# Optimization experiments

Measured on AMD Instinct MI355X. Metric: run time of the kernel, lower is better.

The kernel has to match this reference:

```python
import jax, jax.numpy as jnp
import numpy as np

B, N, DIN, A = 64, 64, 64, 32
DOUT = 128          # obs_output_dim == obs_act_output_dim == 128 (required by module wiring)
OA_IN = DIN + A     # obs_act_input_dim = 96


def _w(key, shape):
    fan_in = shape[-1]
    return jax.random.normal(key, shape, jnp.float32) / jnp.sqrt(jnp.float32(fan_in))


def setup_inputs() -> dict:
    key = jax.random.key(0)
    ks = jax.random.split(key, 14)
    return {
        "states": jax.random.normal(ks[0], (B, N, DIN), jnp.float32),
        "policies": jax.random.uniform(ks[1], (B, N, A), jnp.float32),
        "actions": jax.random.uniform(ks[2], (B, N, A), jnp.float32),
        # state_embed_preproc: Linear(obs_input_dim, 128) + LeakyReLU
        "W_se_pre": _w(ks[3], (128, DIN)),
        "b_se_pre": jnp.zeros((128,), jnp.float32),
        # key/query layers (shared between both attention stages in forward)
        "W_key": _w(ks[4], (DOUT, 128)),
        "W_query": _w(ks[5], (DOUT, 128)),
        # state_embed: Linear(obs_output_dim, 128) + LeakyReLU
        "W_se": _w(ks[6], (128, DOUT)),
        "b_se": jnp.zeros((128,), jnp.float32),
        # state_act_pol_embed: Linear(obs_act_input_dim, 128) + LeakyReLU
        "W_sap": _w(ks[7], (128, OA_IN)),
        "b_sap": jnp.zeros((128,), jnp.float32),
        # attention_value_layer: Linear(128, obs_act_output_dim)
        "W_av": _w(ks[8], (DOUT, 128)),
        # final value head
        "W_f1": _w(ks[9], (64, DOUT)),
        "W_f2": _w(ks[10], (1, 64)),
    }


def reference(states, policies, actions, W_se_pre, b_se_pre, W_key, W_query,
              W_se, b_se, W_sap, b_sap, W_av, W_f1, W_f2):
    lrelu = jax.nn.leaky_relu  # negative_slope=0.01, matches torch default
    d_k = W_key.shape[0]
    inv_sqrt_dk = 1.0 / jnp.sqrt(jnp.asarray(d_k, states.dtype))

    # stage 1: self-attention over agents on raw-state embeddings
    e = lrelu(states @ W_se_pre.T + b_se_pre)                       # [B,N,128]
    q1 = e @ W_query.T
    k1 = e @ W_key.T
    w_pre = jax.nn.softmax(jnp.einsum('bid,bjd->bij', q1, k1) * inv_sqrt_dk, axis=-1)
    # NB: attention_value_layer_preproc output is overwritten in the original forward;
    # the effective value is weight_preproc @ states_embed_preproc.
    av_pre = jnp.einsum('bij,bjd->bid', w_pre, e)                   # [B,N,128]

    # stage 2: self-attention weights over agents on re-embedded states
    se = lrelu(av_pre @ W_se.T + b_se)                              # [B,N,128]
    q2 = se @ W_query.T
    k2 = se @ W_key.T
    w = jax.nn.softmax(jnp.einsum('bid,bjd->bij', q2, k2) * inv_sqrt_dk, axis=-1)

    # obs_actions_policies[b,j,k] = (state_k, policy_k) if j==k else (state_k, action_k)
    obs_act = jnp.concatenate([states, actions], axis=-1)           # [B,N,OA_IN]
    obs_pol = jnp.concatenate([states, policies], axis=-1)
    n = states.shape[1]
    eye = jnp.eye(n, dtype=states.dtype)[None, :, :, None]          # [1,N,N,1]
    oap = eye * obs_pol[:, None, :, :] + (1.0 - eye) * obs_act[:, None, :, :]  # [B,N,N,OA_IN]

    emb = lrelu(oap @ W_sap.T + b_sap)                              # [B,N,N,128]
    av = emb @ W_av.T                                               # [B,N,N,DOUT]

    # fused form of repeat->weight->sum: node[b,i,j,d] = sum_k w[b,i,k] * av[b,j,k,d]
    node = jnp.einsum('bik,bjkd->bijd', w, av)                      # [B,N,N,DOUT]

    value = lrelu(node @ W_f1.T) @ W_f2.T                           # [B,N,N,1]
    return value, w_pre, w
```

## Files before the change

### kernel.cpp

```cpp
#include <hip/hip_runtime.h>

#define DEVFN __device__ __forceinline__

constexpr int BNN = 64 * 64 * 64;
constexpr float SCALE = 0.08838834764831845f;
constexpr float NSLOPE = 0.01f;

constexpr int OFF_WPRET = 0;
constexpr int OFF_M     = 24576;
constexpr int OFF_WSET  = 40960;
constexpr int OFF_WSAPT = 57344;
constexpr int OFF_WAVT  = 69632;
constexpr int OFF_WF1T  = 86016;
constexpr int OFF_E     = 98304;
constexpr int OFF_Q     = 622592;
constexpr int OFF_ET    = 1146880;
constexpr int OFF_SET   = 1671168;
constexpr int OFF_HA    = 2195456;
constexpr int OFF_HD    = 2719744;


DEVFN void fma4(float (&acc)[4], float a, const float4& bv) {
  acc[0] += a * bv.x; acc[1] += a * bv.y; acc[2] += a * bv.z; acc[3] += a * bv.w;
}
DEVFN void fma2(float (&acc)[2], float a, const float2& bv) {
  acc[0] += a * bv.x; acc[1] += a * bv.y;
}


template<int NT>
DEVFN void st128(int tid, const float* __restrict__ src, float* __restrict__ Bs, int rows) {
  const int n4 = rows * 32;
  for (int idx = tid; idx < n4; idx += NT) {
    const int r = idx >> 5, c = idx & 31;
    *reinterpret_cast<float4*>(&Bs[r * 132 + c * 4]) =
        *reinterpret_cast<const float4*>(&src[r * 128 + c * 4]);
  }
}

template<int NT>
DEVFN void st64r(int tid, const float* __restrict__ src, float* __restrict__ Bs, int rows) {
  const int n4 = rows * 16;
  for (int idx = tid; idx < n4; idx += NT) {
    const int r = idx >> 4, c = idx & 15;
    *reinterpret_cast<float4*>(&Bs[r * 68 + c * 4]) =
        *reinterpret_cast<const float4*>(&src[r * 64 + c * 4]);
  }
}

DEVFN void wrT(int tid, const float* __restrict__ S, float* __restrict__ dst, int rq) {
  const int fr = tid >> 2, a4 = tid & 3;
  float t[4];
#pragma unroll
  for (int i = 0; i < 4; ++i) t[i] = S[(a4 * 4 + i) * 132 + fr];
  float4 v; v.x = t[0]; v.y = t[1]; v.z = t[2]; v.w = t[3];
  *reinterpret_cast<float4*>(&dst[fr * 64 + rq * 16 + a4 * 4]) = v;
}


DEVFN void g1(int tid, const float* __restrict__ A, int lda,
              const float* __restrict__ Bs, int K, float (&acc)[4]) {
  const int c0 = (tid & 31) * 4, rg = tid >> 5;
  const float* __restrict__ Ar = A + rg * lda;
#pragma unroll 4
  for (int k4 = 0; k4 < K; k4 += 4) {
    const float4 a4 = *reinterpret_cast<const float4*>(&Ar[k4]);
    const float4 b0 = *reinterpret_cast<const float4*>(&Bs[(k4 + 0) * 132 + c0]);
    const float4 b1 = *reinterpret_cast<const float4*>(&Bs[(k4 + 1) * 132 + c0]);
    const float4 b2 = *reinterpret_cast<const float4*>(&Bs[(k4 + 2) * 132 + c0]);
    const float4 b3 = *reinterpret_cast<const float4*>(&Bs[(k4 + 3) * 132 + c0]);
    fma4(acc, a4.x, b0); fma4(acc, a4.y, b1); fma4(acc, a4.z, b2); fma4(acc, a4.w, b3);
  }
}

DEVFN void g2A(int tid, const float* __restrict__ A0, const float* __restrict__ A1,
               int lda, const float* __restrict__ Bs, int K,
               float (&a0)[4], float (&a1)[4]) {
  const int c0 = (tid & 31) * 4, rg = tid >> 5;
  const float* __restrict__ X = A0 + rg * lda;
  const float* __restrict__ Y = A1 + rg * lda;
#pragma unroll 2
  for (int k4 = 0; k4 < K; k4 += 4) {
    const float4 x4 = *reinterpret_cast<const float4*>(&X[k4]);
    const float4 y4 = *reinterpret_cast<const float4*>(&Y[k4]);
    const float4 b0 = *reinterpret_cast<const float4*>(&Bs[(k4 + 0) * 132 + c0]);
    const float4 b1 = *reinterpret_cast<const float4*>(&Bs[(k4 + 1) * 132 + c0]);
    const float4 b2 = *reinterpret_cast<const float4*>(&Bs[(k4 + 2) * 132 + c0]);
    const float4 b3 = *reinterpret_cast<const float4*>(&Bs[(k4 + 3) * 132 + c0]);
    fma4(a0, x4.x, b0); fma4(a1, y4.x, b0);
    fma4(a0, x4.y, b1); fma4(a1, y4.y, b1);
    fma4(a0, x4.z, b2); fma4(a1, y4.z, b2);
    fma4(a0, x4.w, b3); fma4(a1, y4.w, b3);
  }
}

DEVFN void gH(int tid, const float* __restrict__ A, int lda,
              const float* __restrict__ Bs, int K, float (&acc)[2]) {
  const int c0 = (tid & 31) * 2, rg = tid >> 5;
  const float* __restrict__ Ar = A + rg * lda;
#pragma unroll 4
  for (int k4 = 0; k4 < K; k4 += 4) {
    const float4 a4 = *reinterpret_cast<const float4*>(&Ar[k4]);
    const float2 b0 = *reinterpret_cast<const float2*>(&Bs[(k4 + 0) * 68 + c0]);
    const float2 b1 = *reinterpret_cast<const float2*>(&Bs[(k4 + 1) * 68 + c0]);
    const float2 b2 = *reinterpret_cast<const float2*>(&Bs[(k4 + 2) * 68 + c0]);
    const float2 b3 = *reinterpret_cast<const float2*>(&Bs[(k4 + 3) * 68 + c0]);
    fma2(acc, a4.x, b0); fma2(acc, a4.y, b1); fma2(acc, a4.z, b2); fma2(acc, a4.w, b3);
  }
}

DEVFN void gH2(int tid, const float* __restrict__ A0, const float* __restrict__ A1,
               int lda, const float* __restrict__ Bs, int K,
               float (&a0)[2], float (&a1)[2]) {
  const int c0 = (tid & 31) * 2, rg = tid >> 5;
  const float* __restrict__ X = A0 + rg * lda;
  const float* __restrict__ Y = A1 + rg * lda;
#pragma unroll 2
  for (int k4 = 0; k4 < K; k4 += 4) {
    const float4 x4 = *reinterpret_cast<const float4*>(&X[k4]);
    const float4 y4 = *reinterpret_cast<const float4*>(&Y[k4]);
    const float2 b0 = *reinterpret_cast<const float2*>(&Bs[(k4 + 0) * 68 + c0]);
    const float2 b1 = *reinterpret_cast<const float2*>(&Bs[(k4 + 1) * 68 + c0]);
    const float2 b2 = *reinterpret_cast<const float2*>(&Bs[(k4 + 2) * 68 + c0]);
    const float2 b3 = *reinterpret_cast<const float2*>(&Bs[(k4 + 3) * 68 + c0]);
    fma2(a0, x4.x, b0); fma2(a1, y4.x, b0);
    fma2(a0, x4.y, b1); fma2(a1, y4.y, b1);
    fma2(a0, x4.z, b2); fma2(a1, y4.z, b2);
    fma2(a0, x4.w, b3); fma2(a1, y4.w, b3);
  }
}

template<bool ACT, bool HASB>
DEVFN void epi(int tid, const float (&acc)[4], float* __restrict__ O, int ldo,
               const float* __restrict__ bias) {
  const int c0 = (tid & 31) * 4, rg = tid >> 5;
  float t[4];
#pragma unroll
  for (int i = 0; i < 4; ++i) {
    float x = acc[i];
    if constexpr (HASB) x += bias[c0 + i];
    if constexpr (ACT) x = (x > 0.f) ? x : NSLOPE * x;
    t[i] = x;
  }
  float4 v; v.x = t[0]; v.y = t[1]; v.z = t[2]; v.w = t[3];
  *reinterpret_cast<float4*>(&O[rg * ldo + c0]) = v;
}


DEVFN void score_full(int tid, const float* __restrict__ Qs,
                      const float* __restrict__ Ks, float (&acc)[2]) {
  const int j = tid & 63, iw = tid >> 6;
#pragma unroll 2
  for (int kt = 0; kt < 128; kt += 8) {
    float qv[2][8];
#pragma unroll
    for (int r = 0; r < 2; ++r) {
      *reinterpret_cast<float4*>(&qv[r][0]) =
          *reinterpret_cast<const float4*>(&Qs[(iw * 2 + r) * 132 + kt]);
      *reinterpret_cast<float4*>(&qv[r][4]) =
          *reinterpret_cast<const float4*>(&Qs[(iw * 2 + r) * 132 + kt + 4]);
    }
#pragma unroll
    for (int kk = 0; kk < 8; ++kk) {
      const float kv = Ks[(kt + kk) * 68 + j];
      acc[0] += qv[0][kk] * kv;
      acc[1] += qv[1][kk] * kv;
    }
  }
}

DEVFN void softmax_write(int tid, float (&acc)[2], float* __restrict__ Wp,
                         float* __restrict__ gout) {
  const int j = tid & 63, iw = tid >> 6;
#pragma unroll
  for (int r = 0; r < 2; ++r) {
    float v = acc[r] * SCALE;
    float m = v;
#pragma unroll
    for (int off = 32; off > 0; off >>= 1) m = fmaxf(m, __shfl_xor(m, off, 64));
    const float p = __expf(v - m);
    float s = p;
#pragma unroll
    for (int off = 32; off > 0; off >>= 1) s += __shfl_xor(s, off, 64);
    const float w = p / s;
    Wp[(iw * 2 + r) * 68 + j] = w;
    gout[(iw * 2 + r) * 64 + j] = w;
  }
}


__global__ __launch_bounds__(512) void WPREP(const float* __restrict__ Wpre,
                                             const float* __restrict__ Wq,
                                             const float* __restrict__ Wkey,
                                             const float* __restrict__ Wse,
                                             const float* __restrict__ Wsap,
                                             const float* __restrict__ Wav,
                                             const float* __restrict__ Wf1,
                                             float* __restrict__ ws) {
  __shared__ float As[16 * 132];
  __shared__ float Bs[64 * 132];
  const int tid = threadIdx.x, bid = blockIdx.x;
  if (bid < 120) {
    const int gt = bid * 512 + tid;
    if (gt < 8192) {
      const int c = gt >> 6, k = gt & 63;
      ws[OFF_WPRET + k * 128 + c] = Wpre[gt];
    } else if (gt < 24576) {
      const int i = gt - 8192, c = i >> 7, k = i & 127;
      ws[OFF_WSET + k * 128 + c] = Wse[i];
    } else if (gt < 36864) {
      const int i = gt - 24576, c = i / 96, k = i - c * 96;
      ws[OFF_WSAPT + k * 128 + c] = Wsap[i];
    } else if (gt < 53248) {
      const int i = gt - 36864, c = i >> 7, k = i & 127;
      ws[OFF_WAVT + k * 128 + c] = Wav[i];
    } else if (gt < 61440) {
      const int i = gt - 53248, c = i >> 7, k = i & 127;
      ws[OFF_WF1T + k * 64 + c] = Wf1[i];
    }
  } else {
    const int r0 = (bid - 120) * 16;
    for (int idx = tid; idx < 2048; idx += 512) {
      const int r = idx & 15, o = idx >> 4;
      As[r * 132 + o] = Wq[o * 128 + r0 + r];
    }
    const int c0 = (tid & 31) * 4, rg = tid >> 5;
    float acc[4] = {};
    for (int h = 0; h < 2; ++h) {
      __syncthreads();
      st128<512>(tid, Wkey + h * 8192, Bs, 64);
      __syncthreads();
#pragma unroll 8
      for (int k = 0; k < 64; ++k) {
        const float4 bv = *reinterpret_cast<const float4*>(&Bs[k * 132 + c0]);
        fma4(acc, As[rg * 132 + h * 64 + k], bv);
      }
    }
    float4 v; v.x = acc[0]; v.y = acc[1]; v.z = acc[2]; v.w = acc[3];
    *reinterpret_cast<float4*>(&ws[OFF_M + (r0 + rg) * 128 + c0]) = v;
  }
}

__global__ __launch_bounds__(512) void P1(const float* __restrict__ states,
                                          const float* __restrict__ policies,
                                          const float* __restrict__ actions,
                                          const float* __restrict__ b_sap,
                                          const float* __restrict__ b_se_pre,
                                          float* __restrict__ ws) {
  __shared__ float S[16 * 68];
  __shared__ float Aa[16 * 36], Ap[16 * 36];
  __shared__ float Ea[16 * 132];
  __shared__ float Ep[16 * 132], Dd[16 * 132], Er[16 * 132];
  __shared__ float Bs[8704];
  const int tid = threadIdx.x;
  const int wid = ((blockIdx.x & 7) << 5) | (blockIdx.x >> 3);
  const int b = wid >> 2, rq = wid & 3;
  const int r0g = b * 64 + rq * 16;

  for (int idx = tid; idx < 1024; idx += 512) {
    const int r = idx >> 6, c = idx & 63;
    S[r * 68 + c] = states[(r0g + r) * 64 + c];
  }
  {
    const int r = tid >> 5, c = tid & 31;
    Aa[r * 36 + c] = actions[(r0g + r) * 32 + c];
    Ap[r * 36 + c] = policies[(r0g + r) * 32 + c];
  }
  st128<512>(tid, ws + OFF_WSAPT, Bs, 64);
  __syncthreads();
  float cm[4] = {};
  g1(tid, S, 68, Bs, 64, cm);
  __syncthreads();
  st128<512>(tid, ws + OFF_WSAPT + 8192, Bs, 32);
  __syncthreads();
  float aa[4] = {cm[0], cm[1], cm[2], cm[3]};
  float ap[4] = {cm[0], cm[1], cm[2], cm[3]};
  g2A(tid, Aa, Ap, 36, Bs, 32, aa, ap);
  epi<true, true>(tid, aa, Ea, 132, b_sap);
  epi<true, true>(tid, ap, Ep, 132, b_sap);
  __syncthreads();
  for (int idx = tid; idx < 2048; idx += 512) {
    const int r = idx >> 7, c = idx & 127;
    Ep[r * 132 + c] -= Ea[r * 132 + c];
  }
  __syncthreads();
  st128<512>(tid, ws + OFF_WAVT, Bs, 64);
  __syncthreads();
  float av[4] = {}, dl[4] = {};
  g2A(tid, Ea, Ep, 132, Bs, 64, av, dl);
  __syncthreads();
  st128<512>(tid, ws + OFF_WAVT + 8192, Bs, 64);
  __syncthreads();
  g2A(tid, Ea + 64, Ep + 64, 132, Bs, 64, av, dl);
  __syncthreads();
  epi<false, false>(tid, av, Ea, 132, nullptr);
  epi<false, false>(tid, dl, Dd, 132, nullptr);
  __syncthreads();
  st64r<512>(tid, ws + OFF_WF1T, Bs, 128);
  __syncthreads();
  float ah[2] = {}, aha[2] = {};
  gH2(tid, Dd, Ea, 132, Bs, 64, ah, aha);
  gH2(tid, Dd + 64, Ea + 64, 132, Bs + 64 * 68, 64, ah, aha);
  {
    const int c0 = (tid & 31) * 2, rg = tid >> 5;
    float2 vh; vh.x = ah[0]; vh.y = ah[1];
    float2 va; va.x = aha[0]; va.y = aha[1];
    *reinterpret_cast<float2*>(&ws[OFF_HD + (r0g + rg) * 64 + c0]) = vh;
    *reinterpret_cast<float2*>(&ws[OFF_HA + (r0g + rg) * 64 + c0]) = va;
  }
  __syncthreads();
  st128<512>(tid, ws + OFF_WPRET, Bs, 64);
  __syncthreads();
  {
    float ae[4] = {};
    g1(tid, S, 68, Bs, 64, ae);
    const int c0 = (tid & 31) * 4, rg = tid >> 5;
    float t[4];
#pragma unroll
    for (int i = 0; i < 4; ++i) {
      float x = ae[i] + b_se_pre[c0 + i];
      t[i] = (x > 0.f) ? x : NSLOPE * x;
    }
    float4 v; v.x = t[0]; v.y = t[1]; v.z = t[2]; v.w = t[3];
    *reinterpret_cast<float4*>(&Er[rg * 132 + c0]) = v;
    *reinterpret_cast<float4*>(&ws[OFF_E + (r0g + rg) * 128 + c0]) = v;
  }
  __syncthreads();
  wrT(tid, Er, ws + OFF_ET + b * 8192, rq);
  st128<512>(tid, ws + OFF_M, Bs, 64);
  __syncthreads();
  float af[4] = {};
  g1(tid, Er, 132, Bs, 64, af);
  __syncthreads();
  st128<512>(tid, ws + OFF_M + 8192, Bs, 64);
  __syncthreads();
  g1(tid, Er + 64, 132, Bs, 64, af);
  epi<false, false>(tid, af, ws + OFF_Q + r0g * 128, 128, nullptr);
}

__global__ __launch_bounds__(512) void P3(const float* __restrict__ b_se,
                                          float* __restrict__ ws,
                                          float* __restrict__ out) {
  __shared__ float Qs[16 * 132];
  __shared__ float Bs[8704];
  __shared__ float Wp[16 * 68], AV[16 * 132], SEr[16 * 132];
  const int tid = threadIdx.x;
  const int wid = ((blockIdx.x & 7) << 5) | (blockIdx.x >> 3);
  const int b = wid >> 2, rq = wid & 3;
  const int r0g = b * 64 + rq * 16;

  {
    const int r = tid >> 5, c = tid & 31;
    *reinterpret_cast<float4*>(&Qs[r * 132 + c * 4]) =
        *reinterpret_cast<const float4*>(&ws[OFF_Q + (r0g + r) * 128 + c * 4]);
  }
  st64r<512>(tid, ws + OFF_ET + b * 8192, Bs, 128);
  __syncthreads();
  float sc[2] = {};
  score_full(tid, Qs, Bs, sc);
  softmax_write(tid, sc, Wp, out + BNN + b * 4096 + rq * 1024);
  __syncthreads();
  st128<512>(tid, ws + OFF_E + b * 8192, Bs, 64);
  __syncthreads();
  {
    float a[4] = {};
    g1(tid, Wp, 68, Bs, 64, a);
    epi<false, false>(tid, a, AV, 132, nullptr);
  }
  __syncthreads();
  st128<512>(tid, ws + OFF_WSET, Bs, 64);
  __syncthreads();
  float as[4] = {};
  g1(tid, AV, 132, Bs, 64, as);
  __syncthreads();
  st128<512>(tid, ws + OFF_WSET + 8192, Bs, 64);
  __syncthreads();
  g1(tid, AV + 64, 132, Bs, 64, as);
  {
    const int c0 = (tid & 31) * 4, rg = tid >> 5;
    float t[4];
#pragma unroll
    for (int i = 0; i < 4; ++i) {
      float x = as[i] + b_se[c0 + i];
      t[i] = (x > 0.f) ? x : NSLOPE * x;
    }
    float4 v; v.x = t[0]; v.y = t[1]; v.z = t[2]; v.w = t[3];
    *reinterpret_cast<float4*>(&SEr[rg * 132 + c0]) = v;
  }
  __syncthreads();
  wrT(tid, SEr, ws + OFF_SET + b * 8192, rq);
  st128<512>(tid, ws + OFF_M, Bs, 64);
  __syncthreads();
  float af[4] = {};
  g1(tid, SEr, 132, Bs, 64, af);
  __syncthreads();
  st128<512>(tid, ws + OFF_M + 8192, Bs, 64);
  __syncthreads();
  g1(tid, SEr + 64, 132, Bs, 64, af);
  epi<false, false>(tid, af, ws + OFF_Q + r0g * 128, 128, nullptr);
}

__global__ __launch_bounds__(512) void P4(const float* __restrict__ Wf2g,
                                          float* __restrict__ ws,
                                          float* __restrict__ out) {
  __shared__ float Qs[16 * 132];
  __shared__ float Bs[8704];
  __shared__ float Wp[16 * 68], Hb[16 * 66];
  __shared__ float Hd[64 * 69];
  __shared__ float Wf2s[64];
  const int tid = threadIdx.x;
  const int wid = ((blockIdx.x & 7) << 5) | (blockIdx.x >> 3);
  const int b = wid >> 2, rq = wid & 3;
  const int r0g = b * 64 + rq * 16;

  for (int idx = tid; idx < 4096; idx += 512)
    Hd[(idx >> 6) * 69 + (idx & 63)] = ws[OFF_HD + b * 4096 + idx];
  if (tid < 64) Wf2s[tid] = Wf2g[tid];
  {
    const int r = tid >> 5, c = tid & 31;
    *reinterpret_cast<float4*>(&Qs[r * 132 + c * 4]) =
        *reinterpret_cast<const float4*>(&ws[OFF_Q + (r0g + r) * 128 + c * 4]);
  }
  st64r<512>(tid, ws + OFF_SET + b * 8192, Bs, 128);
  __syncthreads();
  float sc[2] = {};
  score_full(tid, Qs, Bs, sc);
  softmax_write(tid, sc, Wp, out + 2 * BNN + b * 4096 + rq * 1024);
  __syncthreads();
  st64r<512>(tid, ws + OFF_HA + b * 4096, Bs, 64);
  __syncthreads();
  float ah[2] = {};
  gH(tid, Wp, 68, Bs, 64, ah);
  {
    const int c0 = (tid & 31) * 2, rg = tid >> 5;
    float2 v; v.x = ah[0]; v.y = ah[1];
    *reinterpret_cast<float2*>(&Hb[rg * 66 + c0]) = v;
  }
  __syncthreads();
  const int j = tid & 63, iw = tid >> 6;
  float wv[2], a2[2] = {0.f, 0.f};
#pragma unroll
  for (int r = 0; r < 2; ++r) wv[r] = Wp[(iw * 2 + r) * 68 + j];
  for (int f = 0; f < 64; ++f) {
    const float hdv = Hd[j * 69 + f];
    const float wf = Wf2s[f];
#pragma unroll
    for (int r = 0; r < 2; ++r) {
      float t = Hb[(iw * 2 + r) * 66 + f] + wv[r] * hdv;
      t = (t > 0.f) ? t : NSLOPE * t;
      a2[r] += t * wf;
    }
  }
#pragma unroll
  for (int r = 0; r < 2; ++r)
    out[(r0g + iw * 2 + r) * 64 + j] = a2[r];
}

extern "C" void kernel_launch(void* const* d_in, const int* in_sizes, int n_in,
                              void* d_out, int out_size, void* d_ws, size_t ws_size,
                              hipStream_t stream) {
  const float* states   = (const float*)d_in[0];
  const float* policies = (const float*)d_in[1];
  const float* actions  = (const float*)d_in[2];
  const float* W_se_pre = (const float*)d_in[3];
  const float* b_se_pre = (const float*)d_in[4];
  const float* W_key    = (const float*)d_in[5];
  const float* W_query  = (const float*)d_in[6];
  const float* W_se     = (const float*)d_in[7];
  const float* b_se     = (const float*)d_in[8];
  const float* W_sap    = (const float*)d_in[9];
  const float* b_sap    = (const float*)d_in[10];
  const float* W_av     = (const float*)d_in[11];
  const float* W_f1     = (const float*)d_in[12];
  const float* W_f2     = (const float*)d_in[13];
  float* out = (float*)d_out;
  float* ws  = (float*)d_ws;

  WPREP<<<dim3(128), dim3(512), 0, stream>>>(
      W_se_pre, W_query, W_key, W_se, W_sap, W_av, W_f1, ws);
  P1<<<dim3(256), dim3(512), 0, stream>>>(states, policies, actions, b_sap, b_se_pre, ws);
  P3<<<dim3(256), dim3(512), 0, stream>>>(b_se, ws, out);
  P4<<<dim3(256), dim3(512), 0, stream>>>(W_f2, ws, out);
}
```

Measured before the change: 62.17 us.

## Fuse P3 and P4 kernels using per-batch atomic group barrier

Merges the second-stage attention kernel and the final value kernel into one launch. The four blocks of each batch synchronise through a global atomic counter, spinning until all four have written their transposed SE slice. Q2 now stays in shared memory instead of going through the workspace. This removes one kernel launch and a global round trip. In exchange it adds a memset launch and relies on all 256 blocks being co-resident, otherwise the spin wait can deadlock.

```diff
diff --git a/kernel.cpp b/kernel.cpp
--- a/kernel.cpp
+++ b/kernel.cpp
@@ -7,6 +7,7 @@
 constexpr float NSLOPE = 0.01f;
 
 constexpr int OFF_WPRET = 0;
+constexpr int OFF_CNT   = 8192;
 constexpr int OFF_M     = 24576;
 constexpr int OFF_WSET  = 40960;
 constexpr int OFF_WSAPT = 57344;
@@ -186,6 +187,17 @@
     Wp[(iw * 2 + r) * 68 + j] = w;
     gout[(iw * 2 + r) * 64 + j] = w;
   }
+}
+
+DEVFN void groupbar(unsigned* __restrict__ cnt, int tid) {
+  __syncthreads();
+  if (tid == 0) {
+    __hip_atomic_fetch_add(cnt, 1u, __ATOMIC_RELEASE, __HIP_MEMORY_SCOPE_AGENT);
+    while (__hip_atomic_load(cnt, __ATOMIC_ACQUIRE, __HIP_MEMORY_SCOPE_AGENT) < 4u) {
+      __builtin_amdgcn_s_sleep(2);
+    }
+  }
+  __syncthreads();
 }
 
 
@@ -338,94 +350,84 @@
   epi<false, false>(tid, af, ws + OFF_Q + r0g * 128, 128, nullptr);
 }
 
-__global__ __launch_bounds__(512) void P3(const float* __restrict__ b_se,
-                                          float* __restrict__ ws,
-                                          float* __restrict__ out) {
+__global__ __launch_bounds__(512) void P34(const float* __restrict__ b_se,
+                                           const float* __restrict__ Wf2g,
+                                           float* __restrict__ ws,
+                                           float* __restrict__ out) {
   __shared__ float Qs[16 * 132];
   __shared__ float Bs[8704];
-  __shared__ float Wp[16 * 68], AV[16 * 132], SEr[16 * 132];
-  const int tid = threadIdx.x;
-  const int wid = ((blockIdx.x & 7) << 5) | (blockIdx.x >> 3);
-  const int b = wid >> 2, rq = wid & 3;
-  const int r0g = b * 64 + rq * 16;
-
-  {
-    const int r = tid >> 5, c = tid & 31;
-    *reinterpret_cast<float4*>(&Qs[r * 132 + c * 4]) =
-        *reinterpret_cast<const float4*>(&ws[OFF_Q + (r0g + r) * 128 + c * 4]);
-  }
-  st64r<512>(tid, ws + OFF_ET + b * 8192, Bs, 128);
-  __syncthreads();
-  float sc[2] = {};
-  score_full(tid, Qs, Bs, sc);
-  softmax_write(tid, sc, Wp, out + BNN + b * 4096 + rq * 1024);
-  __syncthreads();
-  st128<512>(tid, ws + OFF_E + b * 8192, Bs, 64);
-  __syncthreads();
-  {
-    float a[4] = {};
-    g1(tid, Wp, 68, Bs, 64, a);
-    epi<false, false>(tid, a, AV, 132, nullptr);
-  }
-  __syncthreads();
-  st128<512>(tid, ws + OFF_WSET, Bs, 64);
-  __syncthreads();
-  float as[4] = {};
-  g1(tid, AV, 132, Bs, 64, as);
-  __syncthreads();
-  st128<512>(tid, ws + OFF_WSET + 8192, Bs, 64);
-  __syncthreads();
-  g1(tid, AV + 64, 132, Bs, 64, as);
-  {
-    const int c0 = (tid & 31) * 4, rg = tid >> 5;
-    float t[4];
-#pragma unroll
-    for (int i = 0; i < 4; ++i) {
-      float x = as[i] + b_se[c0 + i];
-      t[i] = (x > 0.f) ? x : NSLOPE * x;
-    }
-    float4 v; v.x = t[0]; v.y = t[1]; v.z = t[2]; v.w = t[3];
-    *reinterpret_cast<float4*>(&SEr[rg * 132 + c0]) = v;
-  }
-  __syncthreads();
-  wrT(tid, SEr, ws + OFF_SET + b * 8192, rq);
-  st128<512>(tid, ws + OFF_M, Bs, 64);
-  __syncthreads();
-  float af[4] = {};
-  g1(tid, SEr, 132, Bs, 64, af);
-  __syncthreads();
-  st128<512>(tid, ws + OFF_M + 8192, Bs, 64);
-  __syncthreads();
-  g1(tid, SEr + 64, 132, Bs, 64, af);
-  epi<false, false>(tid, af, ws + OFF_Q + r0g * 128, 128, nullptr);
-}
-
-__global__ __launch_bounds__(512) void P4(const float* __restrict__ Wf2g,
-                                          float* __restrict__ ws,
-                                          float* __restrict__ out) {
-  __shared__ float Qs[16 * 132];
-  __shared__ float Bs[8704];
-  __shared__ float Wp[16 * 68], Hb[16 * 66];
+  __shared__ float Wp[16 * 68];
+  __shared__ float AV[16 * 132];
+  __shared__ float SEr[16 * 132];
   __shared__ float Hd[64 * 69];
+  __shared__ float Hb[16 * 66];
   __shared__ float Wf2s[64];
   const int tid = threadIdx.x;
   const int wid = ((blockIdx.x & 7) << 5) | (blockIdx.x >> 3);
   const int b = wid >> 2, rq = wid & 3;
   const int r0g = b * 64 + rq * 16;
-
+  unsigned* cnt = (unsigned*)(ws + OFF_CNT) + b;
+
+  {
+    const int r = tid >> 5, c = tid & 31;
+    *reinterpret_cast<float4*>(&Qs[r * 132 + c * 4]) =
+        *reinterpret_cast<const float4*>(&ws[OFF_Q + (r0g + r) * 128 + c * 4]);
+  }
   for (int idx = tid; idx < 4096; idx += 512)
     Hd[(idx >> 6) * 69 + (idx & 63)] = ws[OFF_HD + b * 4096 + idx];
   if (tid < 64) Wf2s[tid] = Wf2g[tid];
-  {
-    const int r = tid >> 5, c = tid & 31;
-    *reinterpret_cast<float4*>(&Qs[r * 132 + c * 4]) =
-        *reinterpret_cast<const float4*>(&ws[OFF_Q + (r0g + r) * 128 + c * 4]);
-  }
-  st64r<512>(tid, ws + OFF_SET + b * 8192, Bs, 128);
+  st64r<512>(tid, ws + OFF_ET + b * 8192, Bs, 128);
   __syncthreads();
   float sc[2] = {};
   score_full(tid, Qs, Bs, sc);
-  softmax_write(tid, sc, Wp, out + 2 * BNN + b * 4096 + rq * 1024);
+  softmax_write(tid, sc, Wp, out + BNN + b * 4096 + rq * 1024);
+  __syncthreads();
+  st128<512>(tid, ws + OFF_E + b * 8192, Bs, 64);
+  __syncthreads();
+  {
+    float a[4] = {};
+    g1(tid, Wp, 68, Bs, 64, a);
+    epi<false, false>(tid, a, AV, 132, nullptr);
+  }
+  __syncthreads();
+  st128<512>(tid, ws + OFF_WSET, Bs, 64);
+  __syncthreads();
+  float as[4] = {};
+  g1(tid, AV, 132, Bs, 64, as);
+  __syncthreads();
+  st128<512>(tid, ws + OFF_WSET + 8192, Bs, 64);
+  __syncthreads();
+  g1(tid, AV + 64, 132, Bs, 64, as);
+  {
+    const int c0 = (tid & 31) * 4, rg = tid >> 5;
+    float t[4];
+#pragma unroll
+    for (int i = 0; i < 4; ++i) {
+      float x = as[i] + b_se[c0 + i];
+      t[i] = (x > 0.f) ? x : NSLOPE * x;
+    }
+    float4 v; v.x = t[0]; v.y = t[1]; v.z = t[2]; v.w = t[3];
+    *reinterpret_cast<float4*>(&SEr[rg * 132 + c0]) = v;
+  }
+  __syncthreads();
+  wrT(tid, SEr, ws + OFF_SET + b * 8192, rq);
+  st128<512>(tid, ws + OFF_M, Bs, 64);
+  __syncthreads();
+  float af[4] = {};
+  g1(tid, SEr, 132, Bs, 64, af);
+  __syncthreads();
+  st128<512>(tid, ws + OFF_M + 8192, Bs, 64);
+  __syncthreads();
+  g1(tid, SEr + 64, 132, Bs, 64, af);
+  epi<false, false>(tid, af, Qs, 132, nullptr);
+
+  groupbar(cnt, tid);
+
+  st64r<512>(tid, ws + OFF_SET + b * 8192, Bs, 128);
+  __syncthreads();
+  float sc2[2] = {};
+  score_full(tid, Qs, Bs, sc2);
+  softmax_write(tid, sc2, Wp, out + 2 * BNN + b * 4096 + rq * 1024);
   __syncthreads();
   st64r<512>(tid, ws + OFF_HA + b * 4096, Bs, 64);
   __syncthreads();
@@ -476,9 +478,9 @@
   float* out = (float*)d_out;
   float* ws  = (float*)d_ws;
 
+  hipMemsetAsync(ws + OFF_CNT, 0, 64 * sizeof(unsigned), stream);
   WPREP<<<dim3(128), dim3(512), 0, stream>>>(
       W_se_pre, W_query, W_key, W_se, W_sap, W_av, W_f1, ws);
   P1<<<dim3(256), dim3(512), 0, stream>>>(states, policies, actions, b_sap, b_se_pre, ws);
-  P3<<<dim3(256), dim3(512), 0, stream>>>(b_se, ws, out);
-  P4<<<dim3(256), dim3(512), 0, stream>>>(W_f2, ws, out);
-}
+  P34<<<dim3(256), dim3(512), 0, stream>>>(b_se, W_f2, ws, out);
+}
```

New measurement: 71.42 us. 14.9% more time.
